# Kernel optimization log

Measured on AMD Instinct MI355X. Metric: run time of the kernel, lower is better.

The kernel has to match this reference:

```python
import jax, jax.numpy as jnp
import numpy as np

NUM_HEADS = 12
STEP_SIZE = 3

def softmax_1(a):
    # exp(a_i) / (1 + sum_j exp(a_j)), numerically stable
    m = jnp.maximum(jnp.max(a, axis=-1, keepdims=True), 0.0)
    e = jnp.exp(a - m)
    return e / (jnp.exp(-m) + jnp.sum(e, axis=-1, keepdims=True))

def setup_inputs() -> dict:
    key = jax.random.key(0)
    ks = jax.random.split(key, 7)
    B, N, C, L = 16, 4096, 768, 16
    s = C ** -0.5
    return {
        "x": jax.random.normal(ks[0], (B, N, C), dtype=jnp.float32),
        "query": jax.random.normal(ks[1], (1, L, C), dtype=jnp.float32),
        "Wq": jax.random.normal(ks[2], (C, C), dtype=jnp.float32) * s,
        "Wk": jax.random.normal(ks[3], (C, C), dtype=jnp.float32) * s,
        "Wv": jax.random.normal(ks[4], (C, C), dtype=jnp.float32) * s,
        "Wproj": jax.random.normal(ks[5], (C, C), dtype=jnp.float32) * s,
        "b_proj": jnp.zeros((C,), dtype=jnp.float32),
    }

def reference(x, query, Wq, Wk, Wv, Wproj, b_proj):
    B, N, C = x.shape
    H = NUM_HEADS
    hd = C // H
    L = query.shape[1]
    scale = hd ** -0.5
    # learned queries broadcast over batch
    queries = jnp.broadcast_to(query, (B, L, C))
    q = (queries @ Wq.T).reshape(B, L, H, hd).transpose(0, 2, 1, 3)  # [B,H,L,hd]
    k = (x @ Wk.T).reshape(B, N, H, hd).transpose(0, 2, 1, 3)        # [B,H,N,hd]
    v = k  # Hopfield update: state retrieves against stored patterns k
    for _ in range(STEP_SIZE):
        qs = q * scale
        attn = jnp.einsum('bhld,bhnd->bhln', qs, k)  # [B,H,L,N]
        attn = softmax_1(attn)
        q = jnp.einsum('bhln,bhnd->bhld', attn, v)   # [B,H,L,hd]
    out = q.transpose(0, 2, 1, 3).reshape(B, L, C)
    out = out @ Wv.T          # self.v output projection (no bias)
    out = out @ Wproj.T + b_proj  # self.proj
    return out
```

## Files before the change

kernel.cpp:

```cpp
#include <hip/hip_runtime.h>


typedef float  float4v  __attribute__((ext_vector_type(4)));
typedef short  short4v  __attribute__((ext_vector_type(4)));
typedef short  short8v  __attribute__((ext_vector_type(8)));
typedef unsigned int uint4v __attribute__((ext_vector_type(4)));
typedef short8v bf16x8;

#define NC 16

__device__ __forceinline__ unsigned short f2bf_hi(float f){
  unsigned int u = __float_as_uint(f);
  u += 0x7fffu + ((u >> 16) & 1u);
  return (unsigned short)(u >> 16);
}
__device__ __forceinline__ float bf2f(unsigned short h){
  return __uint_as_float(((unsigned int)h) << 16);
}
__device__ __forceinline__ unsigned int packbf(float v){
  unsigned short hh = f2bf_hi(v);
  return (unsigned)hh | ((unsigned)f2bf_hi(v - bf2f(hh)) << 16);
}

__global__ __launch_bounds__(256)
void cvt_planar_kernel(const float* __restrict__ src, unsigned short* __restrict__ dh,
                       unsigned short* __restrict__ dl){
  size_t idx = (size_t)blockIdx.x*256 + threadIdx.x;
  float4v v = ((const float4v*)src)[idx];
  short4v h4, l4;
  #pragma unroll
  for(int e=0;e<4;e++){
    unsigned short hh = f2bf_hi(v[e]);
    h4[e] = (short)hh;
    l4[e] = (short)f2bf_hi(v[e] - bf2f(hh));
  }
  ((short4v*)dh)[idx] = h4;
  ((short4v*)dl)[idx] = l4;
}

__global__ __launch_bounds__(256)
void q0_kernel(const float* __restrict__ query, const float* __restrict__ wq,
               float* __restrict__ q0){
  int idx = blockIdx.x*256 + threadIdx.x;
  int l = idx / 768, c = idx - l*768;
  const float* qr = query + l*768;
  const float* wr = wq + (size_t)c*768;
  float s = 0.f;
  for(int j=0;j<768;j+=4){
    float4v a  = *(const float4v*)(qr+j);
    float4v w4 = *(const float4v*)(wr+j);
    s += a[0]*w4[0]+a[1]*w4[1]+a[2]*w4[2]+a[3]*w4[3];
  }
  q0[idx] = s;
}

__global__ __launch_bounds__(256, 3)
void gemm_k_kernel(const float* __restrict__ x, const unsigned short* __restrict__ wh,
                   const unsigned short* __restrict__ wl, unsigned int* __restrict__ kout){
  __shared__ unsigned short Ah[128*40], Al[128*40];
  const int tid  = threadIdx.x;
  const int id   = blockIdx.x;
  const int xcd  = id & 7, slot = id >> 3;
  const int bml  = slot / 6;
  const int bn   = slot - bml*6;
  const int bm   = xcd*64 + bml;
  const int wave = tid >> 6, lane = tid & 63, quad = lane >> 4, l16 = lane & 15;

  float4v acc[8][2];
  #pragma unroll
  for(int i=0;i<8;i++)
    #pragma unroll
    for(int j=0;j<2;j++) acc[i][j] = (float4v){0.f,0.f,0.f,0.f};

  const float* xA = x + (size_t)bm*128*768;
  const unsigned short* wbh = wh + (size_t)(bn*128 + wave*32 + l16)*768 + quad*8;
  const unsigned short* wbl = wl + (size_t)(bn*128 + wave*32 + l16)*768 + quad*8;

  for(int k0=0;k0<768;k0+=32){
    bf16x8 b_h[2], b_l[2];
    #pragma unroll
    for(int j=0;j<2;j++){
      b_h[j] = *(const bf16x8*)(wbh + (size_t)j*16*768 + k0);
      b_l[j] = *(const bf16x8*)(wbl + (size_t)j*16*768 + k0);
    }
    __syncthreads();
    #pragma unroll
    for(int i=0;i<2;i++){
      int fi = tid + i*256;
      int row = fi >> 2, c8 = fi & 3;
      const float* sp = xA + (size_t)row*768 + k0 + c8*8;
      float4v va = *(const float4v*)sp;
      float4v vb = *(const float4v*)(sp + 4);
      short8v hv, lv;
      #pragma unroll
      for(int e=0;e<4;e++){
        unsigned short hh = f2bf_hi(va[e]);
        hv[e] = (short)hh; lv[e] = (short)f2bf_hi(va[e] - bf2f(hh));
        unsigned short hh2 = f2bf_hi(vb[e]);
        hv[e+4] = (short)hh2; lv[e+4] = (short)f2bf_hi(vb[e] - bf2f(hh2));
      }
      *(short8v*)(Ah + row*40 + c8*8) = hv;
      *(short8v*)(Al + row*40 + c8*8) = lv;
    }
    __syncthreads();

    #pragma unroll
    for(int i=0;i<8;i++){
      const int ar = i*16 + l16;
      bf16x8 a_h = *(const bf16x8*)(Ah + ar*40 + quad*8);
      bf16x8 a_l = *(const bf16x8*)(Al + ar*40 + quad*8);
      #pragma unroll
      for(int j=0;j<2;j++){
        acc[i][j] = __builtin_amdgcn_mfma_f32_16x16x32_bf16(a_h, b_h[j], acc[i][j],0,0,0);
        acc[i][j] = __builtin_amdgcn_mfma_f32_16x16x32_bf16(a_l, b_h[j], acc[i][j],0,0,0);
        acc[i][j] = __builtin_amdgcn_mfma_f32_16x16x32_bf16(a_h, b_l[j], acc[i][j],0,0,0);
      }
    }
  }
  const size_t cbase = (size_t)(bm*128)*768 + bn*128 + wave*32;
  #pragma unroll
  for(int i=0;i<8;i++)
    #pragma unroll
    for(int j=0;j<2;j++)
      #pragma unroll
      for(int r=0;r<4;r++)
        kout[cbase + (size_t)(i*16 + quad*4 + r)*768 + j*16 + l16] = packbf(acc[i][j][r]);
}

__global__ __launch_bounds__(256, 6)
void attn_step_kernel(const unsigned int* __restrict__ kbuf, const float* __restrict__ qsrc,
                      long qb_stride, float* __restrict__ qacc, float* __restrict__ lacc){
  __shared__ unsigned int knd[64*68];
  __shared__ float p_s[16*68];
  __shared__ float red[4][16];

  const int tid  = threadIdx.x;
  const int c    = blockIdx.x;
  const int h    = blockIdx.y;
  const int b    = blockIdx.z;
  const int wave = tid >> 6, lane = tid & 63, quad = lane >> 4, l16 = lane & 15;

  const unsigned int* kb = kbuf + ((size_t)b*4096 + (size_t)c*(4096/NC))*768 + h*64;

  const float* qp = qsrc + (size_t)b*qb_stride + (size_t)l16*768 + h*64;
  bf16x8 qh[2], ql[2];
  #pragma unroll
  for(int s = 0; s < 2; ++s){
    float4v v0 = *(const float4v*)(qp + s*32 + quad*8);
    float4v v1 = *(const float4v*)(qp + s*32 + quad*8 + 4);
    #pragma unroll
    for(int e = 0; e < 8; ++e){
      float v = (e < 4 ? v0[e] : v1[e-4]) * 0.125f;
      unsigned short hh = f2bf_hi(v);
      qh[s][e] = (short)hh;
      ql[s][e] = (short)f2bf_hi(v - bf2f(hh));
    }
  }

  float4v acc = (float4v){0.f,0.f,0.f,0.f};
  float lsum = 0.f;

  const int sn = tid >> 2;
  const int dq = tid & 3;

  for(int t = 0; t < (4096/NC)/64; ++t){
    const unsigned int* src = kb + (size_t)(t*64 + sn)*768 + dq*16;
    #pragma unroll
    for(int g = 0; g < 4; ++g){
      *(uint4v*)(knd + sn*68 + dq*16 + g*4) = *(const uint4v*)(src + g*4);
    }
    __syncthreads();

    float4v sfr = (float4v){0.f,0.f,0.f,0.f};
    #pragma unroll
    for(int s = 0; s < 2; ++s){
      const unsigned int* ap = knd + (wave*16 + l16)*68 + s*32 + quad*8;
      uint4v w0 = *(const uint4v*)ap;
      uint4v w1 = *(const uint4v*)(ap + 4);
      bf16x8 a_h, a_l;
      #pragma unroll
      for(int j = 0; j < 4; ++j){
        a_h[j]   = (short)(w0[j] & 0xffffu);  a_l[j]   = (short)(w0[j] >> 16);
        a_h[j+4] = (short)(w1[j] & 0xffffu);  a_l[j+4] = (short)(w1[j] >> 16);
      }
      sfr = __builtin_amdgcn_mfma_f32_16x16x32_bf16(a_h, qh[s], sfr, 0,0,0);
      sfr = __builtin_amdgcn_mfma_f32_16x16x32_bf16(a_l, qh[s], sfr, 0,0,0);
      sfr = __builtin_amdgcn_mfma_f32_16x16x32_bf16(a_h, ql[s], sfr, 0,0,0);
    }
    float4v p;
    #pragma unroll
    for(int r = 0; r < 4; ++r) p[r] = __expf(sfr[r]);
    lsum += p[0] + p[1] + p[2] + p[3];
    *(float4v*)(p_s + l16*68 + wave*16 + quad*4) = p;
    __syncthreads();

    #pragma unroll
    for(int s = 0; s < 2; ++s){
      const float* pp = p_s + l16*68 + s*32 + quad*8;
      float4v p0 = *(const float4v*)pp;
      float4v p1 = *(const float4v*)(pp + 4);
      bf16x8 pa_h, pa_l;
      #pragma unroll
      for(int e = 0; e < 8; ++e){
        float v = (e < 4 ? p0[e] : p1[e-4]);
        unsigned short hh = f2bf_hi(v);
        pa_h[e] = (short)hh;
        pa_l[e] = (short)f2bf_hi(v - bf2f(hh));
      }
      const unsigned int* bp = knd + (size_t)(s*32 + quad*8)*68 + wave*16 + l16;
      bf16x8 kb_h, kb_l;
      #pragma unroll
      for(int j = 0; j < 8; ++j){
        unsigned int w = bp[j*68];
        kb_h[j] = (short)(w & 0xffffu);
        kb_l[j] = (short)(w >> 16);
      }
      acc = __builtin_amdgcn_mfma_f32_16x16x32_bf16(pa_h, kb_h, acc, 0,0,0);
      acc = __builtin_amdgcn_mfma_f32_16x16x32_bf16(pa_l, kb_h, acc, 0,0,0);
      acc = __builtin_amdgcn_mfma_f32_16x16x32_bf16(pa_h, kb_l, acc, 0,0,0);
    }
    __syncthreads();
  }

  lsum += __shfl_xor(lsum, 16);
  lsum += __shfl_xor(lsum, 32);
  if(quad == 0) red[wave][l16] = lsum;
  __syncthreads();
  if(tid < 16){
    float tot = red[0][tid] + red[1][tid] + red[2][tid] + red[3][tid];
    atomicAdd(&lacc[(b*12 + h)*16 + tid], tot);
  }
  #pragma unroll
  for(int r = 0; r < 4; ++r){
    atomicAdd(&qacc[(size_t)(b*16 + quad*4 + r)*768 + h*64 + wave*16 + l16], acc[r]);
  }
}

__global__ __launch_bounds__(256)
void attn_norm_kernel(float* __restrict__ qacc, float* __restrict__ lacc,
                      float* __restrict__ qcur){
  __shared__ float lt[16];
  const int bh = blockIdx.x, b = bh/12, h = bh - (bh/12)*12, tid = threadIdx.x;
  if(tid < 16) lt[tid] = 1.f + lacc[bh*16 + tid];
  __syncthreads();
  if(tid < 16) lacc[bh*16 + tid] = 0.f;
  for(int idx = tid; idx < 1024; idx += 256){
    int l = idx >> 6, d = idx & 63;
    size_t a = (size_t)(b*16 + l)*768 + h*64 + d;
    qcur[a] = qacc[a] / lt[l];
    qacc[a] = 0.f;
  }
}

__global__ __launch_bounds__(256)
void proj_kernel(const float* __restrict__ inp, const float* __restrict__ w,
                 const float* __restrict__ bias, float* __restrict__ out){
  __shared__ float rows[4*768];
  const int r0 = blockIdx.x*4;
  const int c  = blockIdx.y*256 + threadIdx.x;
  for(int j = threadIdx.x; j < 4*768; j += 256) rows[j] = inp[(size_t)r0*768 + j];
  __syncthreads();
  const float* wr = w + (size_t)c*768;
  float a0=0.f, a1=0.f, a2=0.f, a3=0.f;
  for(int j=0;j<768;j+=4){
    float4v w4 = *(const float4v*)(wr+j);
    float4v r0v = *(const float4v*)(rows+j);
    float4v r1v = *(const float4v*)(rows+768+j);
    float4v r2v = *(const float4v*)(rows+1536+j);
    float4v r3v = *(const float4v*)(rows+2304+j);
    #pragma unroll
    for(int e=0;e<4;e++){
      a0 += r0v[e]*w4[e]; a1 += r1v[e]*w4[e];
      a2 += r2v[e]*w4[e]; a3 += r3v[e]*w4[e];
    }
  }
  const float bb = bias ? bias[c] : 0.f;
  out[(size_t)(r0+0)*768 + c] = a0 + bb;
  out[(size_t)(r0+1)*768 + c] = a1 + bb;
  out[(size_t)(r0+2)*768 + c] = a2 + bb;
  out[(size_t)(r0+3)*768 + c] = a3 + bb;
}

extern "C" void kernel_launch(void* const* d_in, const int* in_sizes, int n_in,
                              void* d_out, int out_size, void* d_ws, size_t ws_size,
                              hipStream_t stream){
  const float* x     = (const float*)d_in[0];
  const float* query = (const float*)d_in[1];
  const float* Wq    = (const float*)d_in[2];
  const float* Wk    = (const float*)d_in[3];
  const float* Wv    = (const float*)d_in[4];
  const float* Wproj = (const float*)d_in[5];
  const float* bproj = (const float*)d_in[6];
  float* out = (float*)d_out;

  char* ws = (char*)d_ws;
  unsigned int*   kbuf = (unsigned int*)(ws);
  float*          qcur = (float*)(ws + 201326592);
  float*          q0   = (float*)(ws + 202113024);
  char*           R    = ws + 202162176;
  unsigned short* wkh  = (unsigned short*)(R);
  unsigned short* wkl  = (unsigned short*)(R + 1179648);
  float*          qacc = (float*)(R);
  float*          lacc = (float*)(R + 786432);
  float*          out1 = (float*)(R);

  cvt_planar_kernel<<<576, 256, 0, stream>>>(Wk, wkh, wkl);
  q0_kernel<<<48, 256, 0, stream>>>(query, Wq, q0);
  gemm_k_kernel<<<3072, 256, 0, stream>>>(x, wkh, wkl, kbuf);

  hipMemsetAsync(qacc, 0, 786432 + 12288, stream);
  dim3 sg(NC, 12, 16);
  attn_step_kernel<<<sg, 256, 0, stream>>>(kbuf, q0,   0,       qacc, lacc);
  attn_norm_kernel<<<192, 256, 0, stream>>>(qacc, lacc, qcur);
  attn_step_kernel<<<sg, 256, 0, stream>>>(kbuf, qcur, 16*768,  qacc, lacc);
  attn_norm_kernel<<<192, 256, 0, stream>>>(qacc, lacc, qcur);
  attn_step_kernel<<<sg, 256, 0, stream>>>(kbuf, qcur, 16*768,  qacc, lacc);
  attn_norm_kernel<<<192, 256, 0, stream>>>(qacc, lacc, qcur);

  proj_kernel<<<dim3(64, 3), 256, 0, stream>>>(qcur, Wv, nullptr, out1);
  proj_kernel<<<dim3(64, 3), 256, 0, stream>>>(out1, Wproj, bproj, out);
}
```

Before: 742.2 us.

## Restructure attention step: register prefetch, per-wave P in registers, fewer chunks

The attention step kernel now stages 128-key tiles and prefetches the next tile into registers while the current one is computed. Each wave keeps its exp scores in registers, laid out so they feed the PV MFMA directly, which removes the p_s shared buffer and one barrier per tile. Each wave now accumulates partial outputs over all 64 head dims, so the atomics per block go up while the chunk count drops from 16 to 4, cutting grid size and atomic traffic. Launch-bound occupancy hints are also retuned for the GEMM and attention kernels. The risks are lower occupancy and fewer blocks, which may underfill the GPU.

```diff
diff --git a/kernel.cpp b/kernel.cpp
--- a/kernel.cpp
+++ b/kernel.cpp
@@ -7,7 +7,7 @@
 typedef unsigned int uint4v __attribute__((ext_vector_type(4)));
 typedef short8v bf16x8;
 
-#define NC 16
+#define NC 4
 
 __device__ __forceinline__ unsigned short f2bf_hi(float f){
   unsigned int u = __float_as_uint(f);
@@ -54,7 +54,7 @@
   q0[idx] = s;
 }
 
-__global__ __launch_bounds__(256, 3)
+__global__ __launch_bounds__(256, 4)
 void gemm_k_kernel(const float* __restrict__ x, const unsigned short* __restrict__ wh,
                    const unsigned short* __restrict__ wl, unsigned int* __restrict__ kout){
   __shared__ unsigned short Ah[128*40], Al[128*40];
@@ -127,11 +127,10 @@
         kout[cbase + (size_t)(i*16 + quad*4 + r)*768 + j*16 + l16] = packbf(acc[i][j][r]);
 }
 
-__global__ __launch_bounds__(256, 6)
+__global__ __launch_bounds__(256, 3)
 void attn_step_kernel(const unsigned int* __restrict__ kbuf, const float* __restrict__ qsrc,
                       long qb_stride, float* __restrict__ qacc, float* __restrict__ lacc){
-  __shared__ unsigned int knd[64*68];
-  __shared__ float p_s[16*68];
+  __shared__ unsigned int knd[128*68];
   __shared__ float red[4][16];
 
   const int tid  = threadIdx.x;
@@ -157,67 +156,87 @@
     }
   }
 
-  float4v acc = (float4v){0.f,0.f,0.f,0.f};
+  float4v acc[4];
+  #pragma unroll
+  for(int j=0;j<4;j++) acc[j] = (float4v){0.f,0.f,0.f,0.f};
   float lsum = 0.f;
 
-  const int sn = tid >> 2;
-  const int dq = tid & 3;
-
-  for(int t = 0; t < (4096/NC)/64; ++t){
-    const unsigned int* src = kb + (size_t)(t*64 + sn)*768 + dq*16;
-    #pragma unroll
-    for(int g = 0; g < 4; ++g){
-      *(uint4v*)(knd + sn*68 + dq*16 + g*4) = *(const uint4v*)(src + g*4);
-    }
+  const int prow = tid >> 1, pcol = (tid & 1)*32;
+  const int T = (4096/NC)/128;
+  uint4v pf[8];
+  {
+    const unsigned int* src = kb + (size_t)prow*768 + pcol;
+    #pragma unroll
+    for(int g=0; g<8; ++g) pf[g] = *(const uint4v*)(src + g*4);
+  }
+
+  const int rA = wave*32 + 8*(l16 >> 2) + (l16 & 3);
+
+  for(int t = 0; t < T; ++t){
+    #pragma unroll
+    for(int g=0; g<8; ++g) *(uint4v*)(knd + prow*68 + pcol + g*4) = pf[g];
     __syncthreads();
-
-    float4v sfr = (float4v){0.f,0.f,0.f,0.f};
+    if(t+1 < T){
+      const unsigned int* src = kb + (size_t)((t+1)*128 + prow)*768 + pcol;
+      #pragma unroll
+      for(int g=0; g<8; ++g) pf[g] = *(const uint4v*)(src + g*4);
+    }
+
+    float4v s1 = (float4v){0.f,0.f,0.f,0.f};
+    float4v s2 = (float4v){0.f,0.f,0.f,0.f};
     #pragma unroll
     for(int s = 0; s < 2; ++s){
-      const unsigned int* ap = knd + (wave*16 + l16)*68 + s*32 + quad*8;
-      uint4v w0 = *(const uint4v*)ap;
-      uint4v w1 = *(const uint4v*)(ap + 4);
-      bf16x8 a_h, a_l;
+      const unsigned int* a1p = knd + rA*68 + s*32 + quad*8;
+      const unsigned int* a2p = a1p + 4*68;
+      uint4v w0 = *(const uint4v*)a1p;
+      uint4v w1 = *(const uint4v*)(a1p + 4);
+      uint4v u0 = *(const uint4v*)a2p;
+      uint4v u1 = *(const uint4v*)(a2p + 4);
+      bf16x8 a1h, a1l, a2h, a2l;
       #pragma unroll
       for(int j = 0; j < 4; ++j){
-        a_h[j]   = (short)(w0[j] & 0xffffu);  a_l[j]   = (short)(w0[j] >> 16);
-        a_h[j+4] = (short)(w1[j] & 0xffffu);  a_l[j+4] = (short)(w1[j] >> 16);
+        a1h[j]   = (short)(w0[j] & 0xffffu);  a1l[j]   = (short)(w0[j] >> 16);
+        a1h[j+4] = (short)(w1[j] & 0xffffu);  a1l[j+4] = (short)(w1[j] >> 16);
+        a2h[j]   = (short)(u0[j] & 0xffffu);  a2l[j]   = (short)(u0[j] >> 16);
+        a2h[j+4] = (short)(u1[j] & 0xffffu);  a2l[j+4] = (short)(u1[j] >> 16);
       }
-      sfr = __builtin_amdgcn_mfma_f32_16x16x32_bf16(a_h, qh[s], sfr, 0,0,0);
-      sfr = __builtin_amdgcn_mfma_f32_16x16x32_bf16(a_l, qh[s], sfr, 0,0,0);
-      sfr = __builtin_amdgcn_mfma_f32_16x16x32_bf16(a_h, ql[s], sfr, 0,0,0);
-    }
-    float4v p;
-    #pragma unroll
-    for(int r = 0; r < 4; ++r) p[r] = __expf(sfr[r]);
-    lsum += p[0] + p[1] + p[2] + p[3];
-    *(float4v*)(p_s + l16*68 + wave*16 + quad*4) = p;
-    __syncthreads();
-
-    #pragma unroll
-    for(int s = 0; s < 2; ++s){
-      const float* pp = p_s + l16*68 + s*32 + quad*8;
-      float4v p0 = *(const float4v*)pp;
-      float4v p1 = *(const float4v*)(pp + 4);
-      bf16x8 pa_h, pa_l;
+      s1 = __builtin_amdgcn_mfma_f32_16x16x32_bf16(a1h, qh[s], s1, 0,0,0);
+      s1 = __builtin_amdgcn_mfma_f32_16x16x32_bf16(a1l, qh[s], s1, 0,0,0);
+      s1 = __builtin_amdgcn_mfma_f32_16x16x32_bf16(a1h, ql[s], s1, 0,0,0);
+      s2 = __builtin_amdgcn_mfma_f32_16x16x32_bf16(a2h, qh[s], s2, 0,0,0);
+      s2 = __builtin_amdgcn_mfma_f32_16x16x32_bf16(a2l, qh[s], s2, 0,0,0);
+      s2 = __builtin_amdgcn_mfma_f32_16x16x32_bf16(a2h, ql[s], s2, 0,0,0);
+    }
+
+    bf16x8 pa_h, pa_l;
+    #pragma unroll
+    for(int e = 0; e < 4; ++e){
+      float v = __expf(s1[e]);
+      lsum += v;
+      unsigned short hh = f2bf_hi(v);
+      pa_h[e] = (short)hh;
+      pa_l[e] = (short)f2bf_hi(v - bf2f(hh));
+      float v2 = __expf(s2[e]);
+      lsum += v2;
+      unsigned short hh2 = f2bf_hi(v2);
+      pa_h[e+4] = (short)hh2;
+      pa_l[e+4] = (short)f2bf_hi(v2 - bf2f(hh2));
+    }
+
+    const unsigned int* bbase = knd + (size_t)(wave*32 + quad*8)*68 + l16;
+    #pragma unroll
+    for(int j = 0; j < 4; ++j){
+      const unsigned int* bp = bbase + j*16;
+      bf16x8 kbh, kbl;
       #pragma unroll
       for(int e = 0; e < 8; ++e){
-        float v = (e < 4 ? p0[e] : p1[e-4]);
-        unsigned short hh = f2bf_hi(v);
-        pa_h[e] = (short)hh;
-        pa_l[e] = (short)f2bf_hi(v - bf2f(hh));
+        unsigned int w = bp[e*68];
+        kbh[e] = (short)(w & 0xffffu);
+        kbl[e] = (short)(w >> 16);
       }
-      const unsigned int* bp = knd + (size_t)(s*32 + quad*8)*68 + wave*16 + l16;
-      bf16x8 kb_h, kb_l;
-      #pragma unroll
-      for(int j = 0; j < 8; ++j){
-        unsigned int w = bp[j*68];
-        kb_h[j] = (short)(w & 0xffffu);
-        kb_l[j] = (short)(w >> 16);
-      }
-      acc = __builtin_amdgcn_mfma_f32_16x16x32_bf16(pa_h, kb_h, acc, 0,0,0);
-      acc = __builtin_amdgcn_mfma_f32_16x16x32_bf16(pa_l, kb_h, acc, 0,0,0);
-      acc = __builtin_amdgcn_mfma_f32_16x16x32_bf16(pa_h, kb_l, acc, 0,0,0);
+      acc[j] = __builtin_amdgcn_mfma_f32_16x16x32_bf16(pa_h, kbh, acc[j], 0,0,0);
+      acc[j] = __builtin_amdgcn_mfma_f32_16x16x32_bf16(pa_l, kbh, acc[j], 0,0,0);
+      acc[j] = __builtin_amdgcn_mfma_f32_16x16x32_bf16(pa_h, kbl, acc[j], 0,0,0);
     }
     __syncthreads();
   }
@@ -231,9 +250,10 @@
     atomicAdd(&lacc[(b*12 + h)*16 + tid], tot);
   }
   #pragma unroll
-  for(int r = 0; r < 4; ++r){
-    atomicAdd(&qacc[(size_t)(b*16 + quad*4 + r)*768 + h*64 + wave*16 + l16], acc[r]);
-  }
+  for(int j = 0; j < 4; ++j)
+    #pragma unroll
+    for(int r = 0; r < 4; ++r)
+      atomicAdd(&qacc[(size_t)(b*16 + quad*4 + r)*768 + h*64 + j*16 + l16], acc[j][r]);
 }
 
 __global__ __launch_bounds__(256)
```

Result: no change. 749.2 us (+0.9%).
